# Optimization experiments

Hardware: AMD Instinct MI355X
Metric: run time of the kernel (lower is better)

The kernel has to match this reference:

```python
import jax, jax.numpy as jnp
import numpy as np

B, S, D, H = 4, 2048, 1024, 16
DK = D // H

def setup_inputs() -> dict:
    key = jax.random.key(0)
    ks = jax.random.split(key, 8)
    query = jax.random.normal(ks[0], (B, S, D), dtype=jnp.float32)
    k_in = jax.random.normal(ks[1], (B, S, D), dtype=jnp.float32)
    v_in = jax.random.normal(ks[2], (B, S, D), dtype=jnp.float32)
    # causal mask: 1 where attending allowed, 0 masked (module masks where mask==0)
    mask = jnp.broadcast_to(jnp.tril(jnp.ones((S, S), dtype=jnp.int32)), (B, S, S))
    s = 1.0 / np.sqrt(D)
    w_q = jax.random.normal(ks[3], (D, D), dtype=jnp.float32) * s
    w_k = jax.random.normal(ks[4], (D, D), dtype=jnp.float32) * s
    w_v = jax.random.normal(ks[5], (D, D), dtype=jnp.float32) * s
    w_o = jax.random.normal(ks[6], (D, D), dtype=jnp.float32) * s
    b_o = jnp.zeros((D,), dtype=jnp.float32)
    return {"query": query, "key": k_in, "value": v_in, "mask": mask,
            "w_q": w_q, "w_k": w_k, "w_v": w_v, "w_o": w_o, "b_o": b_o}

def reference(query, key, value, mask, w_q, w_k, w_v, w_o, b_o):
    b, s, d = query.shape
    # projections (nn.Linear: x @ W.T); weights stored as [out, in]
    Q = (query @ w_q.T).reshape(b, s, H, DK).transpose(0, 2, 1, 3)  # [b,h,s,dk]
    K = (key   @ w_k.T).reshape(b, s, H, DK).transpose(0, 2, 1, 3)
    V = (value @ w_v.T).reshape(b, s, H, DK).transpose(0, 2, 1, 3)
    scores = jnp.einsum('bhqd,bhkd->bhqk', Q, K) / np.sqrt(DK)  # [b,h,s,s]
    m = mask[:, None, :, :]  # broadcast over heads
    scores = jnp.where(m == 0, jnp.float32(-1e9), scores)
    attn = jax.nn.softmax(scores, axis=-1)
    out = jnp.einsum('bhqk,bhkd->bhqd', attn, V)  # [b,h,s,dk]
    out = out.transpose(0, 2, 1, 3).reshape(b, s, d)
    out = out @ w_o.T + b_o
    return (out, attn)
```

## Files before the change

kernel.cpp:

```cpp
#include <hip/hip_runtime.h>
#include <hip/hip_bf16.h>

typedef __attribute__((ext_vector_type(8))) short bf16x8;
typedef __attribute__((ext_vector_type(4))) float f32x4;

constexpr int Bn = 4, Sn = 2048, Dn = 1024, Hn = 16;
constexpr int Mn = Bn * Sn;
constexpr float C_SCALE = 0.18033688f;

static __device__ __forceinline__ unsigned short f2bf(float f) {
  union { float f; unsigned int u; } v; v.f = f;
  unsigned int r = v.u + 0x7fffu + ((v.u >> 16) & 1u);
  return (unsigned short)(r >> 16);
}

static __device__ __forceinline__ unsigned int cvtpk_bf16(float lo, float hi) {
  unsigned int r;
  asm("v_cvt_pk_bf16_f32 %0, %1, %2" : "=v"(r) : "v"(lo), "v"(hi));
  return r;
}

static __device__ __forceinline__ void gload_lds16(const unsigned short* g,
                                                   unsigned short* l) {
  __builtin_amdgcn_global_load_lds(
      (const __attribute__((address_space(1))) unsigned int*)g,
      (__attribute__((address_space(3))) unsigned int*)l,
      16, 0, 0);
}

__global__ __launch_bounds__(256)
void cvt7(const float* __restrict__ q, const float* __restrict__ k,
          const float* __restrict__ v, const float* __restrict__ wq,
          const float* __restrict__ wk, const float* __restrict__ wv,
          const float* __restrict__ wo,
          unsigned short* __restrict__ oq, unsigned short* __restrict__ ok,
          unsigned short* __restrict__ ov, unsigned short* __restrict__ owq,
          unsigned short* __restrict__ owk, unsigned short* __restrict__ owv,
          unsigned short* __restrict__ owo)
{
  constexpr size_t NX = (size_t)Mn * Dn;
  constexpr size_t NW = (size_t)Dn * Dn;
  constexpr size_t total = 3 * NX + 4 * NW;
  size_t e = ((size_t)blockIdx.x * blockDim.x + threadIdx.x) * 4;
  const size_t step = (size_t)gridDim.x * blockDim.x * 4;
  for (; e < total; e += step) {
    int seg; size_t off;
    if (e < 3 * NX) { seg = (int)(e >> 23); off = e & (NX - 1); }
    else { const size_t j = e - 3 * NX; seg = 3 + (int)(j >> 20); off = j & (NW - 1); }
    const float* src; unsigned short* dst;
    switch (seg) {
      case 0: src = q;  dst = oq;  break;
      case 1: src = k;  dst = ok;  break;
      case 2: src = v;  dst = ov;  break;
      case 3: src = wq; dst = owq; break;
      case 4: src = wk; dst = owk; break;
      case 5: src = wv; dst = owv; break;
      default: src = wo; dst = owo; break;
    }
    const float4 val = *(const float4*)(src + off);
    ushort4 o;
    o.x = f2bf(val.x); o.y = f2bf(val.y); o.z = f2bf(val.z); o.w = f2bf(val.w);
    *(ushort4*)(dst + off) = o;
  }
}

static __device__ __forceinline__ void gemm_core(
    const unsigned short* __restrict__ A, const unsigned short* __restrict__ Bw,
    unsigned short* Asl, unsigned short* Bsl,
    int m0, int n0, int wave, int lane, f32x4 (*acc)[4])
{
  const int lr = lane & 15, lg = lane >> 4;
  const int wm = wave >> 1, wn = wave & 1;
  const int srow = wave * 32 + (lane >> 2);
  const int scol = (lane & 3) * 8;
  const unsigned short* ga0 = A  + (size_t)(m0 + srow) * 1024 + scol;
  const unsigned short* gb0 = Bw + (size_t)(n0 + srow) * 1024 + scol;

  for (int k0 = 0; k0 < 1024; k0 += 32) {
    __syncthreads();
    gload_lds16(ga0 + k0,             &Asl[(wave * 32) * 32]);
    gload_lds16(ga0 + k0 + 16 * 1024, &Asl[(wave * 32 + 16) * 32]);
    gload_lds16(gb0 + k0,             &Bsl[(wave * 32) * 32]);
    gload_lds16(gb0 + k0 + 16 * 1024, &Bsl[(wave * 32 + 16) * 32]);
    __syncthreads();

    bf16x8 af[4], bfr[4];
    #pragma unroll
    for (int mf = 0; mf < 4; ++mf)
      af[mf] = *(const bf16x8*)&Asl[(wm * 64 + mf * 16 + lr) * 32 + lg * 8];
    #pragma unroll
    for (int nf = 0; nf < 4; ++nf)
      bfr[nf] = *(const bf16x8*)&Bsl[(wn * 64 + nf * 16 + lr) * 32 + lg * 8];
    #pragma unroll
    for (int mf = 0; mf < 4; ++mf)
      #pragma unroll
      for (int nf = 0; nf < 4; ++nf)
        acc[mf][nf] = __builtin_amdgcn_mfma_f32_16x16x32_bf16(
            af[mf], bfr[nf], acc[mf][nf], 0, 0, 0);
  }
}

__global__ __launch_bounds__(256)
void gemm_qkv(const unsigned short* __restrict__ Xq,
              const unsigned short* __restrict__ Xk,
              const unsigned short* __restrict__ Xv,
              const unsigned short* __restrict__ Wq,
              const unsigned short* __restrict__ Wk,
              const unsigned short* __restrict__ Wv,
              unsigned short* __restrict__ Qbf,
              unsigned short* __restrict__ Kbf,
              unsigned short* __restrict__ Vtb)
{
  __shared__ unsigned short Asl[128 * 32];
  __shared__ unsigned short Bsl[128 * 32];
  __shared__ unsigned short Ts[128][136];

  const int tid  = threadIdx.x;
  const int wave = tid >> 6, lane = tid & 63;
  const int lr = lane & 15, lg = lane >> 4;
  const int wm = wave >> 1, wn = wave & 1;
  const int m0 = blockIdx.x * 128;
  const int n0 = blockIdx.y * 128;
  const int z  = blockIdx.z;

  const unsigned short* A  = (z == 0) ? Xq : (z == 1) ? Xk : Xv;
  const unsigned short* Bw = (z == 0) ? Wq : (z == 1) ? Wk : Wv;

  f32x4 acc[4][4] = {};
  gemm_core(A, Bw, Asl, Bsl, m0, n0, wave, lane, acc);

  if (z < 2) {
    unsigned short* C = (z == 0) ? Qbf : Kbf;
    const float cs = (z == 0) ? C_SCALE : 1.0f;
    #pragma unroll
    for (int mf = 0; mf < 4; ++mf)
      #pragma unroll
      for (int nf = 0; nf < 4; ++nf)
        #pragma unroll
        for (int i = 0; i < 4; ++i) {
          const int row = m0 + wm * 64 + mf * 16 + lg * 4 + i;
          const int col = n0 + wn * 64 + nf * 16 + lr;
          C[(size_t)row * 1024 + col] = f2bf(acc[mf][nf][i] * cs);
        }
  } else {
    #pragma unroll
    for (int mf = 0; mf < 4; ++mf)
      #pragma unroll
      for (int nf = 0; nf < 4; ++nf)
        #pragma unroll
        for (int i = 0; i < 4; ++i)
          Ts[wn * 64 + nf * 16 + lr][wm * 64 + mf * 16 + lg * 4 + i] =
              f2bf(acc[mf][nf][i]);
    __syncthreads();
    const int dkl = tid >> 1;
    const int sh  = (tid & 1) * 64;
    const int b = m0 >> 11, s0 = m0 & 2047;
    const int gcol = n0 + dkl;
    const int h = gcol >> 6, dk = gcol & 63;
    unsigned short* dst =
        Vtb + ((size_t)((b * 16 + h) * 64 + dk)) * Sn + s0 + sh;
    #pragma unroll
    for (int jj = 0; jj < 8; ++jj)
      *(bf16x8*)(dst + jj * 8) = *(const bf16x8*)&Ts[dkl][sh + jj * 8];
  }
}

__global__ __launch_bounds__(256)
void gemm_o(const unsigned short* __restrict__ A,
            const unsigned short* __restrict__ Bw,
            float* __restrict__ C, const float* __restrict__ bias)
{
  __shared__ unsigned short Asl[128 * 32];
  __shared__ unsigned short Bsl[128 * 32];
  const int tid  = threadIdx.x;
  const int wave = tid >> 6, lane = tid & 63;
  const int lr = lane & 15, lg = lane >> 4;
  const int wm = wave >> 1, wn = wave & 1;
  const int m0 = blockIdx.x * 128;
  const int n0 = blockIdx.y * 128;

  f32x4 acc[4][4] = {};
  gemm_core(A, Bw, Asl, Bsl, m0, n0, wave, lane, acc);

  float bv[4];
  #pragma unroll
  for (int nf = 0; nf < 4; ++nf) bv[nf] = bias[n0 + wn * 64 + nf * 16 + lr];
  #pragma unroll
  for (int mf = 0; mf < 4; ++mf)
    #pragma unroll
    for (int nf = 0; nf < 4; ++nf)
      #pragma unroll
      for (int i = 0; i < 4; ++i) {
        const int row = m0 + wm * 64 + mf * 16 + lg * 4 + i;
        const int col = n0 + wn * 64 + nf * 16 + lr;
        C[(size_t)row * 1024 + col] = acc[mf][nf][i] + bv[nf];
      }
}

__global__ __launch_bounds__(128)
void attn_fused(const unsigned short* __restrict__ Qb,
                const unsigned short* __restrict__ Kb,
                const unsigned short* __restrict__ Vt,
                float* __restrict__ attn_out,
                unsigned short* __restrict__ Ob)
{
  __shared__ unsigned short Ps[2][16][88];

  const int tid = threadIdx.x;
  const int w = tid >> 6, lane = tid & 63;
  const int lr = lane & 15, lg = lane >> 4;
  const int bh = blockIdx.x >> 6;
  const int j  = blockIdx.x & 63;
  const int qs = w ? (127 - j) : j;
  const int b = bh >> 4, h = bh & 15;
  const int q0 = qs * 16;
  const int nkt = (q0 + 15) / 64 + 1;
  const int kl  = nkt - 1;

  const unsigned short* Kbh = Kb + (size_t)(b * Sn) * Dn + h * 64;
  const unsigned short* Vbh = Vt + (size_t)(bh * 64) * Sn;
  float* aout = attn_out + (size_t)bh * Sn * (size_t)Sn;

  const int q = q0 + lr;
  const int qoff = (b * Sn + q) * Dn + h * 64 + lg * 8;
  bf16x8 qf[2];
  qf[0] = *(const bf16x8*)(Qb + qoff);
  qf[1] = *(const bf16x8*)(Qb + qoff + 32);

  float l = 0.f;

  for (int kt = 0; kt < kl; ++kt) {
    bf16x8 kf[4][2];
    #pragma unroll
    for (int nf = 0; nf < 4; ++nf)
      #pragma unroll
      for (int kk = 0; kk < 2; ++kk)
        kf[nf][kk] = *(const bf16x8*)(
            Kbh + (kt * 64 + nf * 16 + lr) * Dn + kk * 32 + lg * 8);
    #pragma unroll
    for (int nf = 0; nf < 4; ++nf) {
      f32x4 a = {0.f, 0.f, 0.f, 0.f};
      a = __builtin_amdgcn_mfma_f32_16x16x32_bf16(kf[nf][0], qf[0], a, 0, 0, 0);
      a = __builtin_amdgcn_mfma_f32_16x16x32_bf16(kf[nf][1], qf[1], a, 0, 0, 0);
      l += (exp2f(a[0]) + exp2f(a[1])) + (exp2f(a[2]) + exp2f(a[3]));
    }
  }
  {
    bf16x8 kf[4][2];
    #pragma unroll
    for (int nf = 0; nf < 4; ++nf)
      #pragma unroll
      for (int kk = 0; kk < 2; ++kk)
        kf[nf][kk] = *(const bf16x8*)(
            Kbh + (kl * 64 + nf * 16 + lr) * Dn + kk * 32 + lg * 8);
    #pragma unroll
    for (int nf = 0; nf < 4; ++nf) {
      f32x4 a = {0.f, 0.f, 0.f, 0.f};
      a = __builtin_amdgcn_mfma_f32_16x16x32_bf16(kf[nf][0], qf[0], a, 0, 0, 0);
      a = __builtin_amdgcn_mfma_f32_16x16x32_bf16(kf[nf][1], qf[1], a, 0, 0, 0);
      #pragma unroll
      for (int i = 0; i < 4; ++i) {
        const int key = kl * 64 + nf * 16 + lg * 4 + i;
        l += (key <= q) ? exp2f(a[i]) : 0.f;
      }
    }
  }
  l += __shfl_xor(l, 16, 64);
  l += __shfl_xor(l, 32, 64);
  const float nlg = -log2f(l);

  f32x4 oacc[4] = {};
  for (int kt = 0; kt < nkt; ++kt) {
    const bool last = (kt == kl);
    bf16x8 kf[4][2], vt[4][2];
    #pragma unroll
    for (int nf = 0; nf < 4; ++nf)
      #pragma unroll
      for (int kk = 0; kk < 2; ++kk) {
        kf[nf][kk] = *(const bf16x8*)(
            Kbh + (kt * 64 + nf * 16 + lr) * Dn + kk * 32 + lg * 8);
        vt[nf][kk] = *(const bf16x8*)(
            Vbh + (nf * 16 + lr) * Sn + kt * 64 + kk * 32 + lg * 8);
      }
    #pragma unroll
    for (int nf = 0; nf < 4; ++nf) {
      f32x4 a = {0.f, 0.f, 0.f, 0.f};
      a = __builtin_amdgcn_mfma_f32_16x16x32_bf16(kf[nf][0], qf[0], a, 0, 0, 0);
      a = __builtin_amdgcn_mfma_f32_16x16x32_bf16(kf[nf][1], qf[1], a, 0, 0, 0);
      f32x4 p4;
      if (!last) {
        #pragma unroll
        for (int i = 0; i < 4; ++i) p4[i] = exp2f(a[i] + nlg);
      } else {
        #pragma unroll
        for (int i = 0; i < 4; ++i) {
          const int key = kl * 64 + nf * 16 + lg * 4 + i;
          const float v = exp2f(a[i] + nlg);
          p4[i] = (key <= q) ? v : 0.f;
        }
      }
      __builtin_nontemporal_store(
          p4, (f32x4*)&aout[q * Sn + kt * 64 + nf * 16 + lg * 4]);
      uint2 pk;
      pk.x = cvtpk_bf16(p4[0], p4[1]);
      pk.y = cvtpk_bf16(p4[2], p4[3]);
      *(uint2*)&Ps[w][lr][nf * 16 + lg * 4] = pk;
    }
    bf16x8 pa[2];
    pa[0] = *(const bf16x8*)&Ps[w][lr][lg * 8];
    pa[1] = *(const bf16x8*)&Ps[w][lr][32 + lg * 8];
    #pragma unroll
    for (int kk = 0; kk < 2; ++kk)
      #pragma unroll
      for (int nf = 0; nf < 4; ++nf)
        oacc[nf] = __builtin_amdgcn_mfma_f32_16x16x32_bf16(
            pa[kk], vt[nf][kk], oacc[nf], 0, 0, 0);
  }
  for (int kt = nkt; kt < Sn / 64; ++kt) {
    const f32x4 z = {0.f, 0.f, 0.f, 0.f};
    #pragma unroll
    for (int jj = 0; jj < 4; ++jj) {
      const int r = q0 + lg + 4 * jj;
      __builtin_nontemporal_store(
          z, (f32x4*)&aout[r * Sn + kt * 64 + lr * 4]);
    }
  }
  #pragma unroll
  for (int nf = 0; nf < 4; ++nf)
    #pragma unroll
    for (int i = 0; i < 4; ++i) {
      const int qq = q0 + lg * 4 + i;
      const int dk = nf * 16 + lr;
      Ob[(b * Sn + qq) * Dn + h * 64 + dk] = f2bf(oacc[nf][i]);
    }
}

extern "C" void kernel_launch(void* const* d_in, const int* in_sizes, int n_in,
                              void* d_out, int out_size, void* d_ws, size_t ws_size,
                              hipStream_t stream)
{
  const float* query = (const float*)d_in[0];
  const float* key   = (const float*)d_in[1];
  const float* value = (const float*)d_in[2];
  const float* w_q = (const float*)d_in[4];
  const float* w_k = (const float*)d_in[5];
  const float* w_v = (const float*)d_in[6];
  const float* w_o = (const float*)d_in[7];
  const float* b_o = (const float*)d_in[8];

  constexpr size_t NX = (size_t)Mn * Dn;
  constexpr size_t NW = (size_t)Dn * Dn;
  unsigned short* Xq  = (unsigned short*)d_ws;
  unsigned short* Xk  = Xq  + NX;
  unsigned short* Xv  = Xk  + NX;
  unsigned short* Wq  = Xv  + NX;
  unsigned short* Wk  = Wq  + NW;
  unsigned short* Wv  = Wk  + NW;
  unsigned short* Wo  = Wv  + NW;
  unsigned short* Qbf = Wo  + NW;
  unsigned short* Kbf = Qbf + NX;
  unsigned short* Vtb = Kbf + NX;
  unsigned short* Obf = Vtb + NX;

  float* out  = (float*)d_out;
  float* attn = out + NX;

  cvt7<<<dim3(2048), dim3(256), 0, stream>>>(query, key, value, w_q, w_k, w_v, w_o,
                                             Xq, Xk, Xv, Wq, Wk, Wv, Wo);
  gemm_qkv<<<dim3(Mn / 128, Dn / 128, 3), dim3(256), 0, stream>>>(
      Xq, Xk, Xv, Wq, Wk, Wv, Qbf, Kbf, Vtb);
  attn_fused<<<dim3(64 * 64), dim3(128), 0, stream>>>(Qbf, Kbf, Vtb, attn, Obf);
  gemm_o<<<dim3(Mn / 128, Dn / 128), dim3(256), 0, stream>>>(Obf, Wo, out, b_o);
}
```

Measured before the change: 564.4 us.

## Double GEMM K-tile to 64 with XOR-swizzled LDS layout and aliased shared buffer

The shared GEMM core now stages a 64-wide K slice per iteration instead of 32, halving the number of barrier pairs per output tile. The LDS layout is XOR-swizzled on 16-byte chunks so the MFMA fragment reads avoid bank conflicts. In the QKV kernel the staging buffers are aliased with the V-transpose scratch to keep LDS usage from growing, which needs an extra barrier before the transpose. The doubled LDS footprint in gemm_o may reduce occupancy.

```diff
diff --git a/kernel.cpp b/kernel.cpp
--- a/kernel.cpp
+++ b/kernel.cpp
@@ -69,34 +69,41 @@
     unsigned short* Asl, unsigned short* Bsl,
     int m0, int n0, int wave, int lane, f32x4 (*acc)[4])
 {
+  const int tid = wave * 64 + lane;
   const int lr = lane & 15, lg = lane >> 4;
   const int wm = wave >> 1, wn = wave & 1;
-  const int srow = wave * 32 + (lane >> 2);
-  const int scol = (lane & 3) * 8;
-  const unsigned short* ga0 = A  + (size_t)(m0 + srow) * 1024 + scol;
-  const unsigned short* gb0 = Bw + (size_t)(n0 + srow) * 1024 + scol;
-
-  for (int k0 = 0; k0 < 1024; k0 += 32) {
+
+  for (int k0 = 0; k0 < 1024; k0 += 64) {
     __syncthreads();
-    gload_lds16(ga0 + k0,             &Asl[(wave * 32) * 32]);
-    gload_lds16(ga0 + k0 + 16 * 1024, &Asl[(wave * 32 + 16) * 32]);
-    gload_lds16(gb0 + k0,             &Bsl[(wave * 32) * 32]);
-    gload_lds16(gb0 + k0 + 16 * 1024, &Bsl[(wave * 32 + 16) * 32]);
+    #pragma unroll
+    for (int it = 0; it < 4; ++it) {
+      const int e = it * 256 + tid;
+      const int row = e >> 3;
+      const int col = ((e & 7) ^ (row & 7)) * 8;
+      gload_lds16(A  + (size_t)(m0 + row) * 1024 + k0 + col,
+                  &Asl[(it * 256 + wave * 64) * 8]);
+      gload_lds16(Bw + (size_t)(n0 + row) * 1024 + k0 + col,
+                  &Bsl[(it * 256 + wave * 64) * 8]);
+    }
     __syncthreads();
 
-    bf16x8 af[4], bfr[4];
-    #pragma unroll
-    for (int mf = 0; mf < 4; ++mf)
-      af[mf] = *(const bf16x8*)&Asl[(wm * 64 + mf * 16 + lr) * 32 + lg * 8];
-    #pragma unroll
-    for (int nf = 0; nf < 4; ++nf)
-      bfr[nf] = *(const bf16x8*)&Bsl[(wn * 64 + nf * 16 + lr) * 32 + lg * 8];
-    #pragma unroll
-    for (int mf = 0; mf < 4; ++mf)
+    #pragma unroll
+    for (int kk = 0; kk < 2; ++kk) {
+      const int ch = ((kk * 4 + lg) ^ (lr & 7)) * 8;
+      bf16x8 af[4], bfr[4];
+      #pragma unroll
+      for (int mf = 0; mf < 4; ++mf)
+        af[mf] = *(const bf16x8*)&Asl[(wm * 64 + mf * 16 + lr) * 64 + ch];
       #pragma unroll
       for (int nf = 0; nf < 4; ++nf)
-        acc[mf][nf] = __builtin_amdgcn_mfma_f32_16x16x32_bf16(
-            af[mf], bfr[nf], acc[mf][nf], 0, 0, 0);
+        bfr[nf] = *(const bf16x8*)&Bsl[(wn * 64 + nf * 16 + lr) * 64 + ch];
+      #pragma unroll
+      for (int mf = 0; mf < 4; ++mf)
+        #pragma unroll
+        for (int nf = 0; nf < 4; ++nf)
+          acc[mf][nf] = __builtin_amdgcn_mfma_f32_16x16x32_bf16(
+              af[mf], bfr[nf], acc[mf][nf], 0, 0, 0);
+    }
   }
 }
 
@@ -111,9 +118,9 @@
               unsigned short* __restrict__ Kbf,
               unsigned short* __restrict__ Vtb)
 {
-  __shared__ unsigned short Asl[128 * 32];
-  __shared__ unsigned short Bsl[128 * 32];
-  __shared__ unsigned short Ts[128][136];
+  __shared__ unsigned short ShBuf[128 * 136];
+  unsigned short* Asl = ShBuf;
+  unsigned short* Bsl = ShBuf + 128 * 64;
 
   const int tid  = threadIdx.x;
   const int wave = tid >> 6, lane = tid & 63;
@@ -143,6 +150,8 @@
           C[(size_t)row * 1024 + col] = f2bf(acc[mf][nf][i] * cs);
         }
   } else {
+    unsigned short (*Ts)[136] = (unsigned short (*)[136])ShBuf;
+    __syncthreads();
     #pragma unroll
     for (int mf = 0; mf < 4; ++mf)
       #pragma unroll
@@ -170,8 +179,8 @@
             const unsigned short* __restrict__ Bw,
             float* __restrict__ C, const float* __restrict__ bias)
 {
-  __shared__ unsigned short Asl[128 * 32];
-  __shared__ unsigned short Bsl[128 * 32];
+  __shared__ unsigned short Asl[128 * 64];
+  __shared__ unsigned short Bsl[128 * 64];
   const int tid  = threadIdx.x;
   const int wave = tid >> 6, lane = tid & 63;
   const int lr = lane & 15, lg = lane >> 4;
```

Result: no change. 554.8 us (-1.7%).
